# Kernel optimization log

Measured on AMD Instinct MI355X. Metric: run time of the kernel, lower is better.

## Reference

```python
import jax, jax.numpy as jnp
import numpy as np

EMBED = 768
HEADS = 12
HEAD_DIM = EMBED // HEADS
RATES = (1, 2, 4)
SEGS = (2048, 4096, 8192)


def setup_inputs() -> dict:
    key = jax.random.key(0)
    k1, k2, k3 = jax.random.split(key, 3)
    b, n = 2, 8192
    x = jax.random.normal(k1, (b, n, EMBED), dtype=jnp.float32)
    Wqkv = jax.random.normal(k2, (3 * EMBED, EMBED), dtype=jnp.float32) * 0.02
    Wout = jax.random.normal(k3, (EMBED, EMBED), dtype=jnp.float32) * 0.02
    return {"x": x, "Wqkv": Wqkv, "Wout": Wout}


def _dilated_attention(qkv):
    # qkv: [b, n, 3, h, d]
    b, n, _, h, d = qkv.shape
    scale = 1.0 / jnp.sqrt(jnp.asarray(d, qkv.dtype))
    out = jnp.zeros((b, n, h, d), dtype=qkv.dtype)
    for r, s in zip(RATES, SEGS):
        sr = s // r
        nseg = n // s
        # strided gather: [b, nseg, sr, 3, h, d]
        g = qkv.reshape(b, nseg, s, 3, h, d)[:, :, ::r]
        # fold stride offset into batch; attention runs over the segment axis
        g = g.transpose(0, 2, 1, 3, 4, 5).reshape(b * sr, nseg, 3, h, d)
        q, k, v = g[:, :, 0], g[:, :, 1], g[:, :, 2]
        scores = jnp.einsum('bnhd,bmhd->bhnm', q, k) * scale
        attn = jax.nn.softmax(scores, axis=-1)
        o = jnp.einsum('bhnm,bmhd->bnhd', attn, v)
        # scatter-add back into strided positions
        o = o.reshape(b, sr, nseg, h, d).transpose(0, 2, 1, 3, 4)
        out = out.reshape(b, nseg, s, h, d).at[:, :, ::r].add(o).reshape(b, n, h, d)
    # normalize over full sequence dim (as in original module)
    out = out / out.sum(axis=1, keepdims=True)
    return out


def reference(x, Wqkv, Wout):
    b, n, e = x.shape
    qkv = (x @ Wqkv.T).reshape(b, n, 3, HEADS, HEAD_DIM)
    o = _dilated_attention(qkv)  # [b, n, h, d]
    return o.reshape(b, n, e) @ Wout.T
```

## Files before the change

### kernel.cpp

```cpp
#include <hip/hip_runtime.h>

typedef unsigned short u16;
typedef __attribute__((ext_vector_type(8))) short bf16x8;
typedef __attribute__((ext_vector_type(4))) float f32x4;

__device__ __forceinline__ u16 f2bf_rne(float f) {
  unsigned u = __float_as_uint(f);
  u += 0x7fffu + ((u >> 16) & 1u);
  return (u16)(u >> 16);
}
__device__ __forceinline__ float bf2f(u16 h) {
  return __uint_as_float(((unsigned)h) << 16);
}
__device__ __forceinline__ void split1(float v, u16& h, u16& l) {
  u16 hh = f2bf_rne(v);
  h = hh;
  l = f2bf_rne(v - bf2f(hh));
}

__device__ __forceinline__ void gl16(const void* g, void* l) {
  __builtin_amdgcn_global_load_lds(
      (const __attribute__((address_space(1))) unsigned int*)g,
      (__attribute__((address_space(3))) unsigned int*)l,
      16, 0, 0);
}

__global__ void split_convert_all(const float4* __restrict__ x,
                                  ushort4* __restrict__ xhi, ushort4* __restrict__ xlo,
                                  const float4* __restrict__ wq,
                                  ushort4* __restrict__ wqh, ushort4* __restrict__ wql) {
  int i = blockIdx.x * 256 + threadIdx.x;
  const float4* src;
  ushort4 *dh, *dl;
  int idx;
  if (i < 3145728) { src = x; dh = xhi; dl = xlo; idx = i; }
  else if (i < 3588096) { src = wq; dh = wqh; dl = wql; idx = i - 3145728; }
  else return;
  float4 v = src[idx];
  ushort4 h, l;
  split1(v.x, h.x, l.x); split1(v.y, h.y, l.y);
  split1(v.z, h.z, l.z); split1(v.w, h.w, l.w);
  dh[idx] = h; dl[idx] = l;
}

__global__ __launch_bounds__(256, 2) void gemm_split_bt(
    const u16* __restrict__ Ahi, const u16* __restrict__ Alo, int lda,
    const u16* __restrict__ Bhi, const u16* __restrict__ Blo,
    const u16* __restrict__ Bhi2, const u16* __restrict__ Blo2,
    float* __restrict__ C, int M, int N, int K) {
  __shared__ __align__(16) u16 sAh[128 * 64], sAl[128 * 64], sBh[128 * 64], sBl[128 * 64];
  const int tid = threadIdx.x;
  const int wave = tid >> 6;
  const int lane = tid & 63;
  const int tm0 = blockIdx.x * 128;
  const int tn0 = blockIdx.y * 128;
  const int wm = (wave & 1) * 64;
  const int wn = (wave >> 1) * 64;
  if (2 * tm0 >= M) { Bhi = Bhi2; Blo = Blo2; }

  const int srow = wave * 32 + (lane >> 3);
  const int c = lane & 7;
  const int scol = (c ^ ((lane >> 3) & 7)) * 8;
  const u16* gAh = Ahi + (size_t)(tm0 + srow) * lda + scol;
  const u16* gAl = Alo + (size_t)(tm0 + srow) * lda + scol;
  const u16* gBh = Bhi + (size_t)(tn0 + srow) * K + scol;
  const u16* gBl = Blo + (size_t)(tn0 + srow) * K + scol;
  u16* lAh = &sAh[wave * 32 * 64];
  u16* lAl = &sAl[wave * 32 * 64];
  u16* lBh = &sBh[wave * 32 * 64];
  u16* lBl = &sBl[wave * 32 * 64];
  const size_t rstepA = (size_t)8 * lda;
  const size_t rstepB = (size_t)8 * K;

  f32x4 acc[4][4] = {};
  const int fr = lane & 15;
  const int quad = lane >> 4;

  for (int kt = 0; kt < K; kt += 64) {
#pragma unroll
    for (int r = 0; r < 4; ++r) {
      gl16(gAh + kt + r * rstepA, lAh + r * 512);
      gl16(gAl + kt + r * rstepA, lAl + r * 512);
      gl16(gBh + kt + r * rstepB, lBh + r * 512);
      gl16(gBl + kt + r * rstepB, lBl + r * 512);
    }
    __syncthreads();
    for (int subk = 0; subk < 2; ++subk) {
      const int k0 = ((subk * 4 + quad) ^ (fr & 7)) * 8;
      bf16x8 ah[4], al[4], bh[4], bl[4];
#pragma unroll
      for (int i = 0; i < 4; ++i) {
        ah[i] = *(const bf16x8*)&sAh[(wm + i * 16 + fr) * 64 + k0];
        al[i] = *(const bf16x8*)&sAl[(wm + i * 16 + fr) * 64 + k0];
        bh[i] = *(const bf16x8*)&sBh[(wn + i * 16 + fr) * 64 + k0];
        bl[i] = *(const bf16x8*)&sBl[(wn + i * 16 + fr) * 64 + k0];
      }
#pragma unroll
      for (int i = 0; i < 4; ++i)
#pragma unroll
        for (int j = 0; j < 4; ++j) {
          acc[i][j] = __builtin_amdgcn_mfma_f32_16x16x32_bf16(ah[i], bh[j], acc[i][j], 0, 0, 0);
          acc[i][j] = __builtin_amdgcn_mfma_f32_16x16x32_bf16(ah[i], bl[j], acc[i][j], 0, 0, 0);
          acc[i][j] = __builtin_amdgcn_mfma_f32_16x16x32_bf16(al[i], bh[j], acc[i][j], 0, 0, 0);
        }
    }
    __syncthreads();
  }

  const int col = lane & 15;
  const int rowq = (lane >> 4) * 4;
#pragma unroll
  for (int i = 0; i < 4; ++i)
#pragma unroll
    for (int j = 0; j < 4; ++j) {
      size_t base = (size_t)(tm0 + wm + i * 16 + rowq) * N + (tn0 + wn + j * 16 + col);
#pragma unroll
      for (int r = 0; r < 4; ++r) C[base + (size_t)r * N] = acc[i][j][r];
    }
}

__global__ __launch_bounds__(256) void attn_dilated(const float* __restrict__ qkv,
                                                    u16* __restrict__ qk16,
                                                    float* __restrict__ Spart) {
  __shared__ float rows[4][2312];
  __shared__ float sc[12][16];
  __shared__ float Aw[12][16];
  const int t = threadIdx.x;
  const int i0 = blockIdx.x;
  const int b = blockIdx.y;
  const size_t rowbase = (size_t)b * 8192 + i0;

  for (int idx = t; idx < 4 * 576; idx += 256) {
    int j = idx / 576, c4 = idx - j * 576;
    ((float4*)rows[j])[c4] = ((const float4*)(qkv + (rowbase + 2048 * j) * 2304))[c4];
  }
  __syncthreads();

  if (t < 192) {
    int h = t >> 4, j = (t >> 2) & 3, jp = t & 3;
    const float4* q = (const float4*)&rows[j][h * 64];
    const float4* k = (const float4*)&rows[jp][768 + h * 64];
    float s = 0.f;
#pragma unroll
    for (int d = 0; d < 16; ++d) {
      float4 a = q[d], bb = k[d];
      s += a.x * bb.x + a.y * bb.y + a.z * bb.z + a.w * bb.w;
    }
    sc[h][(j << 2) | jp] = s * 0.125f;
  }
  __syncthreads();

  if (t < 48) {
    int h = t >> 2, j = t & 3;
    float s0 = sc[h][j * 4 + 0], s1 = sc[h][j * 4 + 1];
    float s2 = sc[h][j * 4 + 2], s3 = sc[h][j * 4 + 3];
    float m = fmaxf(fmaxf(s0, s1), fmaxf(s2, s3));
    float e0 = expf(s0 - m), e1 = expf(s1 - m), e2 = expf(s2 - m), e3 = expf(s3 - m);
    float inv = 1.f / (e0 + e1 + e2 + e3);
    float a[4] = {e0 * inv, e1 * inv, e2 * inv, e3 * inv};
    if ((i0 & 1) == 0) {
      int p = j ^ 2;
      float ss = sc[h][j * 4 + j], sx = sc[h][j * 4 + p];
      float mm = fmaxf(ss, sx);
      float es = expf(ss - mm), ex = expf(sx - mm);
      float iv = 1.f / (es + ex);
      a[j] += es * iv;
      a[p] += ex * iv;
    }
    if ((i0 & 3) == 0) a[j] += 1.f;
    Aw[h][j * 4 + 0] = a[0]; Aw[h][j * 4 + 1] = a[1];
    Aw[h][j * 4 + 2] = a[2]; Aw[h][j * 4 + 3] = a[3];
  }
  __syncthreads();

  float* sp = Spart + ((size_t)b * 64 + (i0 & 63)) * 768;
#pragma unroll
  for (int rep = 0; rep < 3; ++rep) {
    int cc = rep * 256 + t;
    int h = cc >> 6;
    float ps = 0.f;
#pragma unroll
    for (int j = 0; j < 4; ++j) {
      float v = 0.f;
#pragma unroll
      for (int jp = 0; jp < 4; ++jp) v = fmaf(Aw[h][(j << 2) | jp], rows[jp][1536 + cc], v);
      u16 h16, l16;
      split1(v, h16, l16);
      size_t base = (rowbase + 2048 * j) * 4608;
      qk16[base + cc] = h16;
      qk16[base + 768 + cc] = l16;
      ps += v;
    }
    atomicAdd(&sp[cc], ps);
  }
}

__global__ void colred(const float* __restrict__ Spart, float* __restrict__ Sinv) {
  int i = blockIdx.x * 256 + threadIdx.x;
  if (i >= 1536) return;
  int b = i / 768, c = i - b * 768;
  const float* p = Spart + (size_t)b * 64 * 768 + c;
  float s = 0.f;
#pragma unroll
  for (int g = 0; g < 64; ++g) s += p[g * 768];
  Sinv[i] = 1.0f / s;
}

__global__ void scale_wout(const float4* __restrict__ Wout, const float* __restrict__ Sinv,
                           ushort4* __restrict__ wh0, ushort4* __restrict__ wl0,
                           ushort4* __restrict__ wh1, ushort4* __restrict__ wl1) {
  int i = blockIdx.x * 256 + threadIdx.x;
  if (i >= 294912) return;
  int b = i / 147456;
  int r = i - b * 147456;
  int c = (r % 192) * 4;
  const float* s = Sinv + b * 768 + c;
  float4 v = Wout[r];
  v.x *= s[0]; v.y *= s[1]; v.z *= s[2]; v.w *= s[3];
  ushort4 h, l;
  split1(v.x, h.x, l.x); split1(v.y, h.y, l.y);
  split1(v.z, h.z, l.z); split1(v.w, h.w, l.w);
  if (b == 0) { wh0[r] = h; wl0[r] = l; }
  else        { wh1[r] = h; wl1[r] = l; }
}

extern "C" void kernel_launch(void* const* d_in, const int* in_sizes, int n_in,
                              void* d_out, int out_size, void* d_ws, size_t ws_size,
                              hipStream_t stream) {
  (void)in_sizes; (void)n_in; (void)out_size; (void)ws_size;
  const float* x = (const float*)d_in[0];
  const float* Wqkv = (const float*)d_in[1];
  const float* Wout = (const float*)d_in[2];
  float* out = (float*)d_out;

  char* w = (char*)d_ws;
  float* qkv = (float*)(w);
  u16* qk16 = (u16*)(w);
  size_t off = 150994944;
  u16* xhi = (u16*)(w + off);
  float* Spart = (float*)(w + off);
  float* Sinv = (float*)(w + off + 393216);
  u16* wh0 = (u16*)(w + off + 400000);
  u16* wl0 = (u16*)(w + off + 1579648);
  u16* wh1 = (u16*)(w + off + 2759296);
  u16* wl1 = (u16*)(w + off + 3938944);
  off += 25165824;
  u16* xlo = (u16*)(w + off); off += 25165824;
  u16* wqh = (u16*)(w + off); off += 3538944;
  u16* wql = (u16*)(w + off); off += 3538944;

  split_convert_all<<<dim3(14016), 256, 0, stream>>>(
      (const float4*)x, (ushort4*)xhi, (ushort4*)xlo,
      (const float4*)Wqkv, (ushort4*)wqh, (ushort4*)wql);

  gemm_split_bt<<<dim3(128, 18), 256, 0, stream>>>(xhi, xlo, 768, wqh, wql, wqh, wql,
                                                   qkv, 16384, 2304, 768);

  hipMemsetAsync(Spart, 0, 393216, stream);
  attn_dilated<<<dim3(2048, 2), 256, 0, stream>>>(qkv, qk16, Spart);

  colred<<<dim3(6), 256, 0, stream>>>(Spart, Sinv);

  scale_wout<<<dim3(1152), 256, 0, stream>>>((const float4*)Wout, Sinv,
                                             (ushort4*)wh0, (ushort4*)wl0,
                                             (ushort4*)wh1, (ushort4*)wl1);

  gemm_split_bt<<<dim3(128, 6), 256, 0, stream>>>(qk16, qk16 + 768, 4608,
                                                  wh0, wl0, wh1, wl1,
                                                  out, 16384, 768, 768);
}
```

Measured before the change: 370.4 us.

## Double-buffer split-bf16 GEMM LDS tiles with async prefetch two tiles ahead

The split-precision GEMM now stages K-tiles of 32 into two LDS buffers with global_load_lds, prefetching tile t+2 while the MFMAs for tile t run. The full __syncthreads is replaced by explicit vmcnt/lgkmcnt waits and raw barriers, and wave priority is raised around the MFMA block. The goal is to hide global-load latency behind compute in place of the load-then-compute serialisation. In exchange there are twice as many barrier rounds per K, a different XOR swizzle, and hand-written waitcnt counts that must match the number of outstanding loads.

```diff
diff --git a/kernel.cpp b/kernel.cpp
--- a/kernel.cpp
+++ b/kernel.cpp
@@ -48,7 +48,8 @@
     const u16* __restrict__ Bhi, const u16* __restrict__ Blo,
     const u16* __restrict__ Bhi2, const u16* __restrict__ Blo2,
     float* __restrict__ C, int M, int N, int K) {
-  __shared__ __align__(16) u16 sAh[128 * 64], sAl[128 * 64], sBh[128 * 64], sBl[128 * 64];
+  __shared__ __align__(16) u16 sAh[2][128 * 32], sAl[2][128 * 32];
+  __shared__ __align__(16) u16 sBh[2][128 * 32], sBl[2][128 * 32];
   const int tid = threadIdx.x;
   const int wave = tid >> 6;
   const int lane = tid & 63;
@@ -58,53 +59,68 @@
   const int wn = (wave >> 1) * 64;
   if (2 * tm0 >= M) { Bhi = Bhi2; Blo = Blo2; }
 
-  const int srow = wave * 32 + (lane >> 3);
-  const int c = lane & 7;
-  const int scol = (c ^ ((lane >> 3) & 7)) * 8;
-  const u16* gAh = Ahi + (size_t)(tm0 + srow) * lda + scol;
-  const u16* gAl = Alo + (size_t)(tm0 + srow) * lda + scol;
-  const u16* gBh = Bhi + (size_t)(tn0 + srow) * K + scol;
-  const u16* gBl = Blo + (size_t)(tn0 + srow) * K + scol;
-  u16* lAh = &sAh[wave * 32 * 64];
-  u16* lAl = &sAl[wave * 32 * 64];
-  u16* lBh = &sBh[wave * 32 * 64];
-  u16* lBl = &sBl[wave * 32 * 64];
-  const size_t rstepA = (size_t)8 * lda;
-  const size_t rstepB = (size_t)8 * K;
+  const int srow = wave * 32 + (lane >> 2);
+  const int sc = ((lane & 3) ^ ((lane >> 3) & 3)) * 8;
+  const u16* gAh = Ahi + (size_t)(tm0 + srow) * lda + sc;
+  const u16* gAl = Alo + (size_t)(tm0 + srow) * lda + sc;
+  const u16* gBh = Bhi + (size_t)(tn0 + srow) * K + sc;
+  const u16* gBl = Blo + (size_t)(tn0 + srow) * K + sc;
+  const size_t rA = (size_t)16 * lda;
+  const size_t rB = (size_t)16 * K;
+  const int ldst = wave * 1024;
+
+  auto stage = [&](int tile, int b) {
+    const int kk = tile << 5;
+    gl16(gAh + kk, &sAh[b][ldst]);
+    gl16(gAh + kk + rA, &sAh[b][ldst + 512]);
+    gl16(gAl + kk, &sAl[b][ldst]);
+    gl16(gAl + kk + rA, &sAl[b][ldst + 512]);
+    gl16(gBh + kk, &sBh[b][ldst]);
+    gl16(gBh + kk + rB, &sBh[b][ldst + 512]);
+    gl16(gBl + kk, &sBl[b][ldst]);
+    gl16(gBl + kk + rB, &sBl[b][ldst + 512]);
+  };
 
   f32x4 acc[4][4] = {};
   const int fr = lane & 15;
   const int quad = lane >> 4;
-
-  for (int kt = 0; kt < K; kt += 64) {
-#pragma unroll
-    for (int r = 0; r < 4; ++r) {
-      gl16(gAh + kt + r * rstepA, lAh + r * 512);
-      gl16(gAl + kt + r * rstepA, lAl + r * 512);
-      gl16(gBh + kt + r * rstepB, lBh + r * 512);
-      gl16(gBl + kt + r * rstepB, lBl + r * 512);
-    }
-    __syncthreads();
-    for (int subk = 0; subk < 2; ++subk) {
-      const int k0 = ((subk * 4 + quad) ^ (fr & 7)) * 8;
-      bf16x8 ah[4], al[4], bh[4], bl[4];
-#pragma unroll
-      for (int i = 0; i < 4; ++i) {
-        ah[i] = *(const bf16x8*)&sAh[(wm + i * 16 + fr) * 64 + k0];
-        al[i] = *(const bf16x8*)&sAl[(wm + i * 16 + fr) * 64 + k0];
-        bh[i] = *(const bf16x8*)&sBh[(wn + i * 16 + fr) * 64 + k0];
-        bl[i] = *(const bf16x8*)&sBl[(wn + i * 16 + fr) * 64 + k0];
+  const int k0 = (quad ^ ((fr >> 1) & 3)) * 8;
+  const int nt = K >> 5;
+
+  stage(0, 0);
+  stage(1, 1);
+  asm volatile("s_waitcnt vmcnt(8)" ::: "memory");
+  __builtin_amdgcn_s_barrier();
+
+  for (int t = 0; t < nt; ++t) {
+    const int c = t & 1;
+    bf16x8 ah[4], al[4], bh[4], bl[4];
+#pragma unroll
+    for (int i = 0; i < 4; ++i) {
+      ah[i] = *(const bf16x8*)&sAh[c][(wm + i * 16 + fr) * 32 + k0];
+      al[i] = *(const bf16x8*)&sAl[c][(wm + i * 16 + fr) * 32 + k0];
+      bh[i] = *(const bf16x8*)&sBh[c][(wn + i * 16 + fr) * 32 + k0];
+      bl[i] = *(const bf16x8*)&sBl[c][(wn + i * 16 + fr) * 32 + k0];
+    }
+    asm volatile("s_waitcnt lgkmcnt(0)" ::: "memory");
+    __builtin_amdgcn_s_barrier();
+    if (t + 2 < nt) stage(t + 2, c);
+    __builtin_amdgcn_s_setprio(1);
+#pragma unroll
+    for (int i = 0; i < 4; ++i)
+#pragma unroll
+      for (int j = 0; j < 4; ++j) {
+        acc[i][j] = __builtin_amdgcn_mfma_f32_16x16x32_bf16(ah[i], bh[j], acc[i][j], 0, 0, 0);
+        acc[i][j] = __builtin_amdgcn_mfma_f32_16x16x32_bf16(ah[i], bl[j], acc[i][j], 0, 0, 0);
+        acc[i][j] = __builtin_amdgcn_mfma_f32_16x16x32_bf16(al[i], bh[j], acc[i][j], 0, 0, 0);
       }
-#pragma unroll
-      for (int i = 0; i < 4; ++i)
-#pragma unroll
-        for (int j = 0; j < 4; ++j) {
-          acc[i][j] = __builtin_amdgcn_mfma_f32_16x16x32_bf16(ah[i], bh[j], acc[i][j], 0, 0, 0);
-          acc[i][j] = __builtin_amdgcn_mfma_f32_16x16x32_bf16(ah[i], bl[j], acc[i][j], 0, 0, 0);
-          acc[i][j] = __builtin_amdgcn_mfma_f32_16x16x32_bf16(al[i], bh[j], acc[i][j], 0, 0, 0);
-        }
-    }
-    __syncthreads();
+    __builtin_amdgcn_s_setprio(0);
+    if (t + 2 < nt) {
+      asm volatile("s_waitcnt vmcnt(8)" ::: "memory");
+    } else if (t + 1 < nt) {
+      asm volatile("s_waitcnt vmcnt(0)" ::: "memory");
+    }
+    if (t + 1 < nt) __builtin_amdgcn_s_barrier();
   }
 
   const int col = lane & 15;
```

New measurement: 380.9 us. 2.8% more time.
